# Performance work log

Measured on AMD Instinct MI355X. Metric: run time of the kernel, lower is better.

The kernel has to match this reference:

```python
import jax, jax.numpy as jnp
import numpy as np

B, D, L, H, P, IMG = 32, 768, 12, 12, 16, 224
N = (IMG // P) ** 2  # 196 patches
DH = D // H
FF = 4 * D
EPS = 1e-5


def _ln(x, w, b):
    m = jnp.mean(x, axis=-1, keepdims=True)
    v = jnp.mean((x - m) ** 2, axis=-1, keepdims=True)
    return (x - m) * jax.lax.rsqrt(v + EPS) * w + b


def setup_inputs() -> dict:
    key = jax.random.key(0)
    ks = jax.random.split(key, 12)
    s = 0.02
    return {
        "x": jax.random.normal(ks[0], (B, 3, IMG, IMG), jnp.float32),
        "patch_w": jax.random.normal(ks[1], (D, 3, P, P), jnp.float32) * s,
        "patch_b": jnp.zeros((D,), jnp.float32),
        "pos_embed": jax.random.normal(ks[2], (1, N, D), jnp.float32) * s,
        "ln1_w": jnp.ones((L, D), jnp.float32),
        "ln1_b": jnp.zeros((L, D), jnp.float32),
        "qkv_w": jax.random.normal(ks[3], (L, 3 * D, D), jnp.float32) * s,
        "qkv_b": jnp.zeros((L, 3 * D), jnp.float32),
        "proj_w": jax.random.normal(ks[4], (L, D, D), jnp.float32) * s,
        "proj_b": jnp.zeros((L, D), jnp.float32),
        "ln2_w": jnp.ones((L, D), jnp.float32),
        "ln2_b": jnp.zeros((L, D), jnp.float32),
        "fc1_w": jax.random.normal(ks[5], (L, FF, D), jnp.float32) * s,
        "fc1_b": jnp.zeros((L, FF), jnp.float32),
        "fc2_w": jax.random.normal(ks[6], (L, D, FF), jnp.float32) * s,
        "fc2_b": jnp.zeros((L, D), jnp.float32),
        "lnf_w": jnp.ones((D,), jnp.float32),
        "lnf_b": jnp.zeros((D,), jnp.float32),
    }


def reference(x, patch_w, patch_b, pos_embed, ln1_w, ln1_b, qkv_w, qkv_b,
              proj_w, proj_b, ln2_w, ln2_b, fc1_w, fc1_b, fc2_w, fc2_b,
              lnf_w, lnf_b):
    # Patch embed: strided conv, NCHW / OIHW
    h = jax.lax.conv_general_dilated(
        x, patch_w, window_strides=(P, P), padding="VALID",
        dimension_numbers=("NCHW", "OIHW", "NCHW")) + patch_b[None, :, None, None]
    b = h.shape[0]
    h = h.reshape(b, D, -1).transpose(0, 2, 1)  # (B, N, D)
    h = h + pos_embed  # broadcast over batch

    scale = DH ** (-0.5)
    for i in range(L):
        # --- attention (indices=None path: plain masked-free softmax) ---
        y = _ln(h, ln1_w[i], ln1_b[i])
        qkv = y @ qkv_w[i].T + qkv_b[i]                      # (B, N, 3D)
        qkv = qkv.reshape(b, -1, 3, H, DH).transpose(2, 0, 3, 1, 4)
        q, k, v = qkv[0], qkv[1], qkv[2]                     # (B, H, N, DH)
        attn = jax.nn.softmax(jnp.einsum("bhnd,bhmd->bhnm", q, k) * scale, axis=-1)
        o = jnp.einsum("bhnm,bhmd->bhnd", attn, v)
        o = o.transpose(0, 2, 1, 3).reshape(b, -1, D)
        h = h + (o @ proj_w[i].T + proj_b[i])
        # --- MLP ---
        y = _ln(h, ln2_w[i], ln2_b[i])
        y = jax.nn.gelu(y @ fc1_w[i].T + fc1_b[i], approximate=False)
        h = h + (y @ fc2_w[i].T + fc2_b[i])

    return _ln(h, lnf_w, lnf_b)
```

## Files before the change

kernel.cpp:

```cpp
#include <hip/hip_runtime.h>
#include <hip/hip_bf16.h>
#include <math.h>

#define BB    32
#define DD    768
#define LL    12
#define HH    12
#define NN    196
#define DHH   64
#define FFF   3072
#define MM    (BB * NN)
#define BHH   (BB * HH)

typedef float  floatx4 __attribute__((ext_vector_type(4)));
typedef __bf16 bf16x8  __attribute__((ext_vector_type(8)));

#define DEV __device__ __forceinline__

DEV unsigned short bf16u(float v) {
  __hip_bfloat16 h = __float2bfloat16(v);
  return __builtin_bit_cast(unsigned short, h);
}

DEV floatx4 mfma_bf16(bf16x8 a, bf16x8 b, floatx4 c) {
  return __builtin_amdgcn_mfma_f32_16x16x32_bf16(a, b, c, 0, 0, 0);
}

DEV void gl2lds16(const void* g, void* l) {
  __builtin_amdgcn_global_load_lds(
      (const __attribute__((address_space(1))) void*)g,
      (__attribute__((address_space(3))) void*)l, 16, 0, 0);
}

DEV float gelu_f(float v) {
  float ax = fabsf(v) * 0.70710678118654752f;
  float t = 1.0f / (1.0f + 0.3275911f * ax);
  float poly = t * (0.254829592f +
              t * (-0.284496736f +
              t * (1.421413741f +
              t * (-1.453152027f +
              t * 1.061405429f))));
  float er = 1.0f - poly * __expf(-ax * ax);
  er = (v < 0.0f) ? -er : er;
  return 0.5f * v * (1.0f + er);
}

DEV int xcd_swz(int orig, int nwg) {
  int q = nwg >> 3, r = nwg & 7;
  int xcd = orig & 7, pos = orig >> 3;
  int base = (xcd < r) ? xcd * (q + 1) : r * (q + 1) + (xcd - r) * q;
  return base + pos;
}

__global__ __launch_bounds__(256) void cvt4_k(const float4* __restrict__ in,
                                              ushort4* __restrict__ out, int n4) {
  int i = blockIdx.x * 256 + threadIdx.x;
  if (i < n4) {
    float4 v = in[i];
    ushort4 o;
    o.x = bf16u(v.x); o.y = bf16u(v.y); o.z = bf16u(v.z); o.w = bf16u(v.w);
    out[i] = o;
  }
}

__global__ __launch_bounds__(256) void im2col_k(const float* __restrict__ x,
                                                unsigned short* __restrict__ A) {
  int idx = blockIdx.x * 256 + threadIdx.x;
  int col = idx % DD;
  int token = idx / DD;
  int b = token / NN, p = token % NN;
  int pr = p / 14, pc = p % 14;
  int c = col >> 8, rm = col & 255, i = rm >> 4, j = rm & 15;
  float v = x[(((size_t)b * 3 + c) * 224 + pr * 16 + i) * 224 + pc * 16 + j];
  A[idx] = bf16u(v);
}

__global__ __launch_bounds__(256) void ln_k(const float* __restrict__ x,
                                            const float* __restrict__ w,
                                            const float* __restrict__ bb,
                                            unsigned short* __restrict__ outp) {
  const int token = blockIdx.x, tid = threadIdx.x;
  const float* xr = x + (size_t)token * DD;
  float v0 = xr[tid], v1 = xr[tid + 256], v2 = xr[tid + 512];
  float s = v0 + v1 + v2;
  float ss = v0 * v0 + v1 * v1 + v2 * v2;
#pragma unroll
  for (int off = 32; off; off >>= 1) {
    s += __shfl_down(s, off);
    ss += __shfl_down(ss, off);
  }
  __shared__ float rs[4], rq[4];
  if ((tid & 63) == 0) { rs[tid >> 6] = s; rq[tid >> 6] = ss; }
  __syncthreads();
  float tot = rs[0] + rs[1] + rs[2] + rs[3];
  float tq  = rq[0] + rq[1] + rq[2] + rq[3];
  const float mean = tot * (1.0f / 768.0f);
  const float var  = tq * (1.0f / 768.0f) - mean * mean;
  const float rstd = rsqrtf(var + 1e-5f);
#pragma unroll
  for (int t = 0; t < 3; t++) {
    int col = tid + t * 256;
    float xv = (t == 0) ? v0 : (t == 1 ? v1 : v2);
    float yv = (xv - mean) * rstd * w[col] + bb[col];
    outp[(size_t)token * DD + col] = bf16u(yv);
  }
}

template <int FINAL>
__global__ __launch_bounds__(256) void ln_fuse_k(float* __restrict__ h,
    const float* __restrict__ p0, const float* __restrict__ p1,
    const float* __restrict__ w, const float* __restrict__ bb,
    void* __restrict__ outp) {
  const int token = blockIdx.x, tid = threadIdx.x;
  const size_t base = (size_t)token * DD;
  float v[3];
#pragma unroll
  for (int t = 0; t < 3; t++) {
    const int col = tid + t * 256;
    v[t] = h[base + col] + p0[base + col] + p1[base + col];
    if (!FINAL) h[base + col] = v[t];
  }
  float s = v[0] + v[1] + v[2];
  float ss = v[0] * v[0] + v[1] * v[1] + v[2] * v[2];
#pragma unroll
  for (int off = 32; off; off >>= 1) {
    s += __shfl_down(s, off);
    ss += __shfl_down(ss, off);
  }
  __shared__ float rs[4], rq[4];
  if ((tid & 63) == 0) { rs[tid >> 6] = s; rq[tid >> 6] = ss; }
  __syncthreads();
  float tot = rs[0] + rs[1] + rs[2] + rs[3];
  float tq  = rq[0] + rq[1] + rq[2] + rq[3];
  const float mean = tot * (1.0f / 768.0f);
  const float var  = tq * (1.0f / 768.0f) - mean * mean;
  const float rstd = rsqrtf(var + 1e-5f);
#pragma unroll
  for (int t = 0; t < 3; t++) {
    const int col = tid + t * 256;
    float yv = (v[t] - mean) * rstd * w[col] + bb[col];
    if (FINAL) ((float*)outp)[base + col] = yv;
    else       ((unsigned short*)outp)[base + col] = bf16u(yv);
  }
}


template <int MODE>
__global__ __launch_bounds__(256, 4) void gemm_bt(
    const unsigned short* __restrict__ A, const unsigned short* __restrict__ W,
    const float* __restrict__ bias, void* __restrict__ outp, int K, int Nn) {
  __shared__ unsigned short smem[16384];
  unsigned short* As0 = smem;
  unsigned short* Bs0 = smem + 8192;
  const int tid = threadIdx.x;
  const int wave = tid >> 6, lane = tid & 63;
  const int nwg = gridDim.x * gridDim.y;
  const int wg = xcd_swz(blockIdx.x + gridDim.x * blockIdx.y, nwg);
  const int tm = (wg / gridDim.x) * 128, tn = (wg % gridDim.x) * 128;
  const int wm = (wave >> 1) * 64, wn = (wave & 1) * 64;
  const int lr = lane & 15, kq = lane >> 4;
  const int sw = (lr >> 1) & 3;
  const int koff = (kq ^ sw) * 8;
  const int c0 = tid, c1 = tid + 256;
  const int r0 = c0 >> 2, r1 = c1 >> 2;
  const int kc0 = ((c0 & 3) ^ ((r0 >> 1) & 3)) * 8;
  const int kc1 = ((c1 & 3) ^ ((r1 >> 1) & 3)) * 8;
  const size_t ga0 = (size_t)(tm + r0) * K + kc0;
  const size_t ga1 = (size_t)(tm + r1) * K + kc1;
  const size_t gb0 = (size_t)(tn + r0) * K + kc0;
  const size_t gb1 = (size_t)(tn + r1) * K + kc1;
  floatx4 acc[4][4] = {};
  auto stage = [&](int buf, int k0) {
    gl2lds16(A + ga0 + k0, As0 + buf * 4096 + c0 * 8);
    gl2lds16(A + ga1 + k0, As0 + buf * 4096 + c1 * 8);
    gl2lds16(W + gb0 + k0, Bs0 + buf * 4096 + c0 * 8);
    gl2lds16(W + gb1 + k0, Bs0 + buf * 4096 + c1 * 8);
  };
  const int nk = K >> 5;
  stage(0, 0);
  for (int it = 0; it < nk; it++) {
    const int cur = it & 1;
    __syncthreads();
    if (it + 1 < nk) stage(cur ^ 1, (it + 1) << 5);
    bf16x8 af[4], bq[4];
#pragma unroll
    for (int mi = 0; mi < 4; mi++)
      af[mi] = *(const bf16x8*)&As0[cur * 4096 + (wm + mi * 16 + lr) * 32 + koff];
#pragma unroll
    for (int ni = 0; ni < 4; ni++)
      bq[ni] = *(const bf16x8*)&Bs0[cur * 4096 + (wn + ni * 16 + lr) * 32 + koff];
#pragma unroll
    for (int mi = 0; mi < 4; mi++)
#pragma unroll
      for (int ni = 0; ni < 4; ni++)
        acc[mi][ni] = mfma_bf16(af[mi], bq[ni], acc[mi][ni]);
  }
  __syncthreads();
#pragma unroll
  for (int ni = 0; ni < 4; ni++) {
    const int lcol = wn + ni * 16 + lr;
    const float bv = bias[tn + lcol];
#pragma unroll
    for (int mi = 0; mi < 4; mi++) {
#pragma unroll
      for (int r = 0; r < 4; r++) {
        const int lrow = wm + mi * 16 + (lane >> 4) * 4 + r;
        float v = acc[mi][ni][r] + bv;
        if (MODE == 3) v = gelu_f(v);
        smem[lrow * 128 + lcol] = bf16u(v);
      }
    }
  }
  __syncthreads();
  const int tr = tid >> 4;
  const int tc = (tid & 15) * 8;
#pragma unroll
  for (int p = 0; p < 8; p++) {
    const int lrow = p * 16 + tr;
    uint4 d = *(const uint4*)&smem[lrow * 128 + tc];
    *(uint4*)&((unsigned short*)outp)[(size_t)(tm + lrow) * Nn + tn + tc] = d;
  }
}

__global__ __launch_bounds__(256, 4) void gemm_sk(
    const unsigned short* __restrict__ A, const unsigned short* __restrict__ W,
    const float* __restrict__ bias, float* __restrict__ p0,
    float* __restrict__ p1, int K, int Nn) {
  __shared__ unsigned short As[2][128 * 32];
  __shared__ unsigned short Bs[2][128 * 32];
  const int tid = threadIdx.x;
  const int wave = tid >> 6, lane = tid & 63;
  const int nwg = gridDim.x * gridDim.y;
  const int wg = xcd_swz(blockIdx.x + gridDim.x * blockIdx.y, nwg);
  const int tm = (wg / gridDim.x) * 128, tn = (wg % gridDim.x) * 128;
  const int kz = blockIdx.z;
  const int kper = K >> 1;
  const int kbase = kz * kper;
  const int wm = (wave >> 1) * 64, wn = (wave & 1) * 64;
  const int lr = lane & 15, kq = lane >> 4;
  const int sw = (lr >> 1) & 3;
  const int koff = (kq ^ sw) * 8;
  const int c0 = tid, c1 = tid + 256;
  const int r0 = c0 >> 2, r1 = c1 >> 2;
  const int kc0 = ((c0 & 3) ^ ((r0 >> 1) & 3)) * 8;
  const int kc1 = ((c1 & 3) ^ ((r1 >> 1) & 3)) * 8;
  const size_t ga0 = (size_t)(tm + r0) * K + kc0 + kbase;
  const size_t ga1 = (size_t)(tm + r1) * K + kc1 + kbase;
  const size_t gb0 = (size_t)(tn + r0) * K + kc0 + kbase;
  const size_t gb1 = (size_t)(tn + r1) * K + kc1 + kbase;
  floatx4 acc[4][4] = {};
  auto stage = [&](int buf, int k0) {
    gl2lds16(A + ga0 + k0, &As[buf][c0 * 8]);
    gl2lds16(A + ga1 + k0, &As[buf][c1 * 8]);
    gl2lds16(W + gb0 + k0, &Bs[buf][c0 * 8]);
    gl2lds16(W + gb1 + k0, &Bs[buf][c1 * 8]);
  };
  const int nk = kper >> 5;
  stage(0, 0);
  for (int it = 0; it < nk; it++) {
    const int cur = it & 1;
    __syncthreads();
    if (it + 1 < nk) stage(cur ^ 1, (it + 1) << 5);
    bf16x8 af[4], bq[4];
#pragma unroll
    for (int mi = 0; mi < 4; mi++)
      af[mi] = *(const bf16x8*)&As[cur][(wm + mi * 16 + lr) * 32 + koff];
#pragma unroll
    for (int ni = 0; ni < 4; ni++)
      bq[ni] = *(const bf16x8*)&Bs[cur][(wn + ni * 16 + lr) * 32 + koff];
#pragma unroll
    for (int mi = 0; mi < 4; mi++)
#pragma unroll
      for (int ni = 0; ni < 4; ni++)
        acc[mi][ni] = mfma_bf16(af[mi], bq[ni], acc[mi][ni]);
  }
  float* __restrict__ po = kz ? p1 : p0;
  const int rbase = tm + wm + (lane >> 4) * 4;
  const int cbase = tn + wn + lr;
#pragma unroll
  for (int ni = 0; ni < 4; ni++) {
    const int col = cbase + ni * 16;
    const float bv = kz ? 0.0f : bias[col];
#pragma unroll
    for (int mi = 0; mi < 4; mi++) {
#pragma unroll
      for (int r = 0; r < 4; r++) {
        const int row = rbase + mi * 16 + r;
        po[(size_t)row * Nn + col] = acc[mi][ni][r] + bv;
      }
    }
  }
}

template <int MODE>
__global__ __launch_bounds__(256, 4) void gemm64_bt(
    const unsigned short* __restrict__ A, const unsigned short* __restrict__ W,
    const float* __restrict__ bias, const float* __restrict__ aux,
    float* __restrict__ outp, int K, int Nn) {
  __shared__ unsigned short As[2][64 * 32];
  __shared__ unsigned short Bs[2][128 * 32];
  const int tid = threadIdx.x;
  const int wave = tid >> 6, lane = tid & 63;
  const int tm = blockIdx.y * 64, tn = blockIdx.x * 128;
  const int wm = (wave >> 1) * 32, wn = (wave & 1) * 64;
  const int lr = lane & 15, kq = lane >> 4;
  const int sw = (lr >> 1) & 3;
  const int koff = (kq ^ sw) * 8;
  const int ra = tid >> 2;
  const int kca = ((tid & 3) ^ ((ra >> 1) & 3)) * 8;
  const int c0 = tid, c1 = tid + 256;
  const int r0 = c0 >> 2, r1 = c1 >> 2;
  const int kc0 = ((c0 & 3) ^ ((r0 >> 1) & 3)) * 8;
  const int kc1 = ((c1 & 3) ^ ((r1 >> 1) & 3)) * 8;
  const size_t ga  = (size_t)(tm + ra) * K + kca;
  const size_t gb0 = (size_t)(tn + r0) * K + kc0;
  const size_t gb1 = (size_t)(tn + r1) * K + kc1;
  floatx4 acc[2][4] = {};
  auto stage = [&](int buf, int k0) {
    gl2lds16(A + ga + k0, &As[buf][tid * 8]);
    gl2lds16(W + gb0 + k0, &Bs[buf][c0 * 8]);
    gl2lds16(W + gb1 + k0, &Bs[buf][c1 * 8]);
  };
  const int nk = K >> 5;
  stage(0, 0);
  for (int it = 0; it < nk; it++) {
    const int cur = it & 1;
    __syncthreads();
    if (it + 1 < nk) stage(cur ^ 1, (it + 1) << 5);
    bf16x8 af[2], bq[4];
#pragma unroll
    for (int mi = 0; mi < 2; mi++)
      af[mi] = *(const bf16x8*)&As[cur][(wm + mi * 16 + lr) * 32 + koff];
#pragma unroll
    for (int ni = 0; ni < 4; ni++)
      bq[ni] = *(const bf16x8*)&Bs[cur][(wn + ni * 16 + lr) * 32 + koff];
#pragma unroll
    for (int mi = 0; mi < 2; mi++)
#pragma unroll
      for (int ni = 0; ni < 4; ni++)
        acc[mi][ni] = mfma_bf16(af[mi], bq[ni], acc[mi][ni]);
  }
  const int rbase = tm + wm + (lane >> 4) * 4;
  const int cbase = tn + wn + lr;
#pragma unroll
  for (int ni = 0; ni < 4; ni++) {
    const int col = cbase + ni * 16;
    const float bv = bias[col];
#pragma unroll
    for (int mi = 0; mi < 2; mi++) {
#pragma unroll
      for (int r = 0; r < 4; r++) {
        const int row = rbase + mi * 16 + r;
        float v = acc[mi][ni][r] + bv;
        float* hp = outp + (size_t)row * Nn + col;
        if (MODE == 1) *hp = v + aux[(size_t)(row % NN) * Nn + col];
        else           *hp = *hp + v;
      }
    }
  }
}

__global__ __launch_bounds__(256) void attn_fused_k(
    const unsigned short* __restrict__ qkv, const unsigned short* __restrict__ Vt,
    unsigned short* __restrict__ o) {
  __shared__ float S[32][232];
  __shared__ __align__(16) unsigned short Pl[32][232];
  const int tid = threadIdx.x;
  const int bh = blockIdx.x;
  const int b = bh / HH, hh = bh % HH;
  const int i0 = blockIdx.y * 32;
  const int wave = tid >> 6, lane = tid & 63;
  const int lr = lane & 15, k8 = (lane >> 4) * 8;
  for (int t = wave; t < 28; t += 4) {
    const int til = (t / 14) * 16, tj = (t % 14) * 16;
    const int iq = min(i0 + til + lr, NN - 1), jk = min(tj + lr, NN - 1);
    const unsigned short* qb = qkv + (size_t)(b * NN + iq) * 2304 + hh * 64 + k8;
    const unsigned short* kb = qkv + (size_t)(b * NN + jk) * 2304 + 768 + hh * 64 + k8;
    floatx4 acc = {0.f, 0.f, 0.f, 0.f};
    acc = mfma_bf16(*(const bf16x8*)qb, *(const bf16x8*)kb, acc);
    acc = mfma_bf16(*(const bf16x8*)(qb + 32), *(const bf16x8*)(kb + 32), acc);
#pragma unroll
    for (int r = 0; r < 4; r++)
      S[til + (lane >> 4) * 4 + r][tj + lr] = acc[r] * 0.125f;
  }
  __syncthreads();
  const int row = tid >> 3, sub = tid & 7;
  float v[28];
  float m = -1e30f;
#pragma unroll
  for (int t = 0; t < 28; t++) {
    const int c = sub + t * 8;
    v[t] = (c < NN) ? S[row][c] : -1e30f;
    m = fmaxf(m, v[t]);
  }
  m = fmaxf(m, __shfl_xor(m, 1));
  m = fmaxf(m, __shfl_xor(m, 2));
  m = fmaxf(m, __shfl_xor(m, 4));
  float s = 0.f;
#pragma unroll
  for (int t = 0; t < 28; t++) {
    v[t] = (sub + t * 8 < NN) ? __expf(v[t] - m) : 0.f;
    s += v[t];
  }
  s += __shfl_xor(s, 1);
  s += __shfl_xor(s, 2);
  s += __shfl_xor(s, 4);
  const float inv = 1.0f / s;
#pragma unroll
  for (int t = 0; t < 28; t++) Pl[row][sub + t * 8] = bf16u(v[t] * inv);
  __syncthreads();
#pragma unroll
  for (int w = 0; w < 2; w++) {
    const int tt = wave * 2 + w;
    const int it = tt >> 2, dt = tt & 3;
    const unsigned short* vb = Vt + ((size_t)bh * 64 + dt * 16 + lr) * 224 + k8;
    floatx4 acc = {0.f, 0.f, 0.f, 0.f};
#pragma unroll
    for (int k0 = 0; k0 < 224; k0 += 32)
      acc = mfma_bf16(*(const bf16x8*)&Pl[it * 16 + lr][k8 + k0],
                      *(const bf16x8*)(vb + k0), acc);
#pragma unroll
    for (int r = 0; r < 4; r++) {
      const int i = i0 + it * 16 + (lane >> 4) * 4 + r;
      if (i < NN)
        o[(size_t)(b * NN + i) * DD + hh * 64 + dt * 16 + lr] = bf16u(acc[r]);
    }
  }
}

__global__ __launch_bounds__(256) void vt_k(const unsigned short* __restrict__ qkv,
                                            unsigned short* __restrict__ Vt) {
  int idx = blockIdx.x * 256 + threadIdx.x;
  int j = idx % 224;
  int rest = idx / 224;
  int d = rest % 64, bh = rest / 64;
  int b = bh / HH, hh = bh % HH;
  unsigned short val = 0;
  if (j < NN) val = qkv[(size_t)(b * NN + j) * 2304 + 1536 + hh * 64 + d];
  Vt[idx] = val;
}

extern "C" void kernel_launch(void* const* d_in, const int* in_sizes, int n_in,
                              void* d_out, int out_size, void* d_ws, size_t ws_size,
                              hipStream_t stream) {
  const float* x       = (const float*)d_in[0];
  const float* patchw  = (const float*)d_in[1];
  const float* patchb  = (const float*)d_in[2];
  const float* pos     = (const float*)d_in[3];
  const float* ln1w    = (const float*)d_in[4];
  const float* ln1b    = (const float*)d_in[5];
  const float* qkvw    = (const float*)d_in[6];
  const float* qkvb    = (const float*)d_in[7];
  const float* projw   = (const float*)d_in[8];
  const float* projb   = (const float*)d_in[9];
  const float* ln2w    = (const float*)d_in[10];
  const float* ln2b    = (const float*)d_in[11];
  const float* fc1w    = (const float*)d_in[12];
  const float* fc1b    = (const float*)d_in[13];
  const float* fc2w    = (const float*)d_in[14];
  const float* fc2b    = (const float*)d_in[15];
  const float* lnfw    = (const float*)d_in[16];
  const float* lnfb    = (const float*)d_in[17];

  char* base = (char*)d_ws;
  size_t off = 0;
  auto alloc = [&](size_t bytes) {
    void* p = base + off;
    off = (off + bytes + 255) & ~(size_t)255;
    return p;
  };
  unsigned short* Wq  = (unsigned short*)alloc((size_t)LL * 2304 * 768 * 2);
  unsigned short* Wp  = (unsigned short*)alloc((size_t)LL * 768 * 768 * 2);
  unsigned short* W1  = (unsigned short*)alloc((size_t)LL * 3072 * 768 * 2);
  unsigned short* W2  = (unsigned short*)alloc((size_t)LL * 768 * 3072 * 2);
  unsigned short* Wpe = (unsigned short*)alloc((size_t)768 * 768 * 2);
  float*          h   = (float*)alloc((size_t)MM * DD * 4);
  unsigned short* y   = (unsigned short*)alloc((size_t)MM * DD * 2);
  unsigned short* qkv = (unsigned short*)alloc((size_t)MM * 2304 * 2);
  unsigned short* g   = (unsigned short*)alloc((size_t)MM * FFF * 2);
  float*          pp1 = (float*)alloc((size_t)MM * DD * 4);
  unsigned short* Vt  = (unsigned short*)alloc((size_t)BHH * 64 * 224 * 2);
  unsigned short* o   = (unsigned short*)alloc((size_t)MM * DD * 2);
  if (off > ws_size) return;

  unsigned short* Aim = qkv;
  float* pp0 = (float*)qkv;

  auto cvt = [&](const float* src, unsigned short* dst, size_t n) {
    int n4 = (int)(n / 4);
    cvt4_k<<<dim3((n4 + 255) / 256), dim3(256), 0, stream>>>(
        (const float4*)src, (ushort4*)dst, n4);
  };
  cvt(qkvw, Wq, (size_t)LL * 2304 * 768);
  cvt(projw, Wp, (size_t)LL * 768 * 768);
  cvt(fc1w, W1, (size_t)LL * 3072 * 768);
  cvt(fc2w, W2, (size_t)LL * 768 * 3072);
  cvt(patchw, Wpe, (size_t)768 * 768);

  im2col_k<<<dim3(MM * DD / 256), dim3(256), 0, stream>>>(x, Aim);
  gemm64_bt<1><<<dim3(6, 98), dim3(256), 0, stream>>>(Aim, Wpe, patchb, pos, h, 768, 768);

  ln_k<<<dim3(MM), dim3(256), 0, stream>>>(h, ln1w, ln1b, y);

  for (int l = 0; l < LL; l++) {
    gemm_bt<0><<<dim3(18, 49), dim3(256), 0, stream>>>(
        y, Wq + (size_t)l * 2304 * 768, qkvb + l * 2304, qkv, 768, 2304);
    vt_k<<<dim3(BHH * 64 * 224 / 256), dim3(256), 0, stream>>>(qkv, Vt);
    attn_fused_k<<<dim3(BHH, 7), dim3(256), 0, stream>>>(qkv, Vt, o);
    gemm_sk<<<dim3(6, 49, 2), dim3(256), 0, stream>>>(
        o, Wp + (size_t)l * 768 * 768, projb + l * 768, pp0, pp1, 768, 768);
    ln_fuse_k<0><<<dim3(MM), dim3(256), 0, stream>>>(
        h, pp0, pp1, ln2w + l * 768, ln2b + l * 768, y);
    gemm_bt<3><<<dim3(24, 49), dim3(256), 0, stream>>>(
        y, W1 + (size_t)l * 3072 * 768, fc1b + l * 3072, g, 768, 3072);
    gemm_sk<<<dim3(6, 49, 2), dim3(256), 0, stream>>>(
        g, W2 + (size_t)l * 768 * 3072, fc2b + l * 768, pp0, pp1, 3072, 768);
    if (l + 1 < LL) {
      ln_fuse_k<0><<<dim3(MM), dim3(256), 0, stream>>>(
          h, pp0, pp1, ln1w + (l + 1) * 768, ln1b + (l + 1) * 768, y);
    } else {
      ln_fuse_k<1><<<dim3(MM), dim3(256), 0, stream>>>(
          h, pp0, pp1, lnfw, lnfb, d_out);
    }
  }
}
```

Measured before the change: 3.347 ms.

## Fuse V transpose into QKV GEMM epilogue and use wave-per-token layernorm

The QKV GEMM gains a mode whose V-column tiles are transposed in shared memory and written straight into the padded Vt buffer. This removes the separate vt_k transpose kernel each layer, and the zero padding is written once up front. The layernorm kernels now give each token to one wave with float4 loads and xor-shuffle reductions, dropping the shared-memory reduction and block barrier. The trade-offs are a larger LDS footprint in the GEMM, scattered stores for tiles that cross batch boundaries, and partial-qkv writes skipped for V tiles.

```diff
diff --git a/kernel.cpp b/kernel.cpp
--- a/kernel.cpp
+++ b/kernel.cpp
@@ -75,34 +75,49 @@
   A[idx] = bf16u(v);
 }
 
-__global__ __launch_bounds__(256) void ln_k(const float* __restrict__ x,
-                                            const float* __restrict__ w,
-                                            const float* __restrict__ bb,
-                                            unsigned short* __restrict__ outp) {
-  const int token = blockIdx.x, tid = threadIdx.x;
-  const float* xr = x + (size_t)token * DD;
-  float v0 = xr[tid], v1 = xr[tid + 256], v2 = xr[tid + 512];
-  float s = v0 + v1 + v2;
-  float ss = v0 * v0 + v1 * v1 + v2 * v2;
+__global__ __launch_bounds__(256) void vtpad_k(unsigned short* __restrict__ Vt) {
+  int idx = blockIdx.x * 256 + threadIdx.x;
+  int jj = idx % 28, rest = idx / 28;
+  Vt[(size_t)rest * 224 + 196 + jj] = 0;
+}
+
+__global__ __launch_bounds__(256) void lnw_k(const float* __restrict__ x,
+                                             const float* __restrict__ w,
+                                             const float* __restrict__ bb,
+                                             unsigned short* __restrict__ outp) {
+  const int token = blockIdx.x * 4 + (threadIdx.x >> 6);
+  const int lane = threadIdx.x & 63;
+  const size_t base = (size_t)token * DD;
+  const float4* x4 = (const float4*)(x + base);
+  const float4* w4 = (const float4*)w;
+  const float4* b4 = (const float4*)bb;
+  float4 v[3];
+  float s = 0.f, ss = 0.f;
+#pragma unroll
+  for (int j = 0; j < 3; j++) {
+    float4 t = x4[lane + j * 64];
+    v[j] = t;
+    s += t.x + t.y + t.z + t.w;
+    ss += t.x * t.x + t.y * t.y + t.z * t.z + t.w * t.w;
+  }
 #pragma unroll
   for (int off = 32; off; off >>= 1) {
-    s += __shfl_down(s, off);
-    ss += __shfl_down(ss, off);
-  }
-  __shared__ float rs[4], rq[4];
-  if ((tid & 63) == 0) { rs[tid >> 6] = s; rq[tid >> 6] = ss; }
-  __syncthreads();
-  float tot = rs[0] + rs[1] + rs[2] + rs[3];
-  float tq  = rq[0] + rq[1] + rq[2] + rq[3];
-  const float mean = tot * (1.0f / 768.0f);
-  const float var  = tq * (1.0f / 768.0f) - mean * mean;
+    s += __shfl_xor(s, off);
+    ss += __shfl_xor(ss, off);
+  }
+  const float mean = s * (1.0f / 768.0f);
+  const float var  = ss * (1.0f / 768.0f) - mean * mean;
   const float rstd = rsqrtf(var + 1e-5f);
 #pragma unroll
-  for (int t = 0; t < 3; t++) {
-    int col = tid + t * 256;
-    float xv = (t == 0) ? v0 : (t == 1 ? v1 : v2);
-    float yv = (xv - mean) * rstd * w[col] + bb[col];
-    outp[(size_t)token * DD + col] = bf16u(yv);
+  for (int j = 0; j < 3; j++) {
+    const int c4 = lane + j * 64;
+    float4 wv = w4[c4], bv = b4[c4];
+    ushort4 o;
+    o.x = bf16u((v[j].x - mean) * rstd * wv.x + bv.x);
+    o.y = bf16u((v[j].y - mean) * rstd * wv.y + bv.y);
+    o.z = bf16u((v[j].z - mean) * rstd * wv.z + bv.z);
+    o.w = bf16u((v[j].w - mean) * rstd * wv.w + bv.w);
+    ((ushort4*)((unsigned short*)outp + base))[c4] = o;
   }
 }
 
@@ -111,36 +126,52 @@
     const float* __restrict__ p0, const float* __restrict__ p1,
     const float* __restrict__ w, const float* __restrict__ bb,
     void* __restrict__ outp) {
-  const int token = blockIdx.x, tid = threadIdx.x;
+  const int token = blockIdx.x * 4 + (threadIdx.x >> 6);
+  const int lane = threadIdx.x & 63;
   const size_t base = (size_t)token * DD;
-  float v[3];
-#pragma unroll
-  for (int t = 0; t < 3; t++) {
-    const int col = tid + t * 256;
-    v[t] = h[base + col] + p0[base + col] + p1[base + col];
-    if (!FINAL) h[base + col] = v[t];
-  }
-  float s = v[0] + v[1] + v[2];
-  float ss = v[0] * v[0] + v[1] * v[1] + v[2] * v[2];
+  const float4* h4 = (const float4*)(h + base);
+  const float4* p04 = (const float4*)(p0 + base);
+  const float4* p14 = (const float4*)(p1 + base);
+  const float4* w4 = (const float4*)w;
+  const float4* b4 = (const float4*)bb;
+  float4 v[3];
+  float s = 0.f, ss = 0.f;
+#pragma unroll
+  for (int j = 0; j < 3; j++) {
+    const int c4 = lane + j * 64;
+    float4 a = h4[c4], b2 = p04[c4], c2 = p14[c4];
+    float4 t;
+    t.x = a.x + b2.x + c2.x; t.y = a.y + b2.y + c2.y;
+    t.z = a.z + b2.z + c2.z; t.w = a.w + b2.w + c2.w;
+    v[j] = t;
+    s += t.x + t.y + t.z + t.w;
+    ss += t.x * t.x + t.y * t.y + t.z * t.z + t.w * t.w;
+    if (!FINAL) ((float4*)(h + base))[c4] = t;
+  }
 #pragma unroll
   for (int off = 32; off; off >>= 1) {
-    s += __shfl_down(s, off);
-    ss += __shfl_down(ss, off);
-  }
-  __shared__ float rs[4], rq[4];
-  if ((tid & 63) == 0) { rs[tid >> 6] = s; rq[tid >> 6] = ss; }
-  __syncthreads();
-  float tot = rs[0] + rs[1] + rs[2] + rs[3];
-  float tq  = rq[0] + rq[1] + rq[2] + rq[3];
-  const float mean = tot * (1.0f / 768.0f);
-  const float var  = tq * (1.0f / 768.0f) - mean * mean;
+    s += __shfl_xor(s, off);
+    ss += __shfl_xor(ss, off);
+  }
+  const float mean = s * (1.0f / 768.0f);
+  const float var  = ss * (1.0f / 768.0f) - mean * mean;
   const float rstd = rsqrtf(var + 1e-5f);
 #pragma unroll
-  for (int t = 0; t < 3; t++) {
-    const int col = tid + t * 256;
-    float yv = (v[t] - mean) * rstd * w[col] + bb[col];
-    if (FINAL) ((float*)outp)[base + col] = yv;
-    else       ((unsigned short*)outp)[base + col] = bf16u(yv);
+  for (int j = 0; j < 3; j++) {
+    const int c4 = lane + j * 64;
+    float4 wv = w4[c4], bv = b4[c4];
+    float4 yv;
+    yv.x = (v[j].x - mean) * rstd * wv.x + bv.x;
+    yv.y = (v[j].y - mean) * rstd * wv.y + bv.y;
+    yv.z = (v[j].z - mean) * rstd * wv.z + bv.z;
+    yv.w = (v[j].w - mean) * rstd * wv.w + bv.w;
+    if (FINAL) {
+      ((float4*)((float*)outp + base))[c4] = yv;
+    } else {
+      ushort4 o;
+      o.x = bf16u(yv.x); o.y = bf16u(yv.y); o.z = bf16u(yv.z); o.w = bf16u(yv.w);
+      ((ushort4*)((unsigned short*)outp + base))[c4] = o;
+    }
   }
 }
 
@@ -148,8 +179,9 @@
 template <int MODE>
 __global__ __launch_bounds__(256, 4) void gemm_bt(
     const unsigned short* __restrict__ A, const unsigned short* __restrict__ W,
-    const float* __restrict__ bias, void* __restrict__ outp, int K, int Nn) {
-  __shared__ unsigned short smem[16384];
+    const float* __restrict__ bias, void* __restrict__ outp,
+    unsigned short* __restrict__ vtp, int K, int Nn) {
+  __shared__ unsigned short smem[17408];
   unsigned short* As0 = smem;
   unsigned short* Bs0 = smem + 8192;
   const int tid = threadIdx.x;
@@ -196,29 +228,68 @@
         acc[mi][ni] = mfma_bf16(af[mi], bq[ni], acc[mi][ni]);
   }
   __syncthreads();
-#pragma unroll
-  for (int ni = 0; ni < 4; ni++) {
-    const int lcol = wn + ni * 16 + lr;
-    const float bv = bias[tn + lcol];
-#pragma unroll
-    for (int mi = 0; mi < 4; mi++) {
-#pragma unroll
-      for (int r = 0; r < 4; r++) {
-        const int lrow = wm + mi * 16 + (lane >> 4) * 4 + r;
-        float v = acc[mi][ni][r] + bv;
-        if (MODE == 3) v = gelu_f(v);
-        smem[lrow * 128 + lcol] = bf16u(v);
+  const bool vtile = (MODE == 4) && (tn >= 1536);
+  if (vtile) {
+#pragma unroll
+    for (int ni = 0; ni < 4; ni++) {
+      const int lcol = wn + ni * 16 + lr;
+      const float bv = bias[tn + lcol];
+#pragma unroll
+      for (int mi = 0; mi < 4; mi++) {
+#pragma unroll
+        for (int r = 0; r < 4; r++) {
+          const int lrow = wm + mi * 16 + (lane >> 4) * 4 + r;
+          smem[lcol * 136 + lrow] = bf16u(acc[mi][ni][r] + bv);
+        }
       }
     }
-  }
-  __syncthreads();
-  const int tr = tid >> 4;
-  const int tc = (tid & 15) * 8;
-#pragma unroll
-  for (int p = 0; p < 8; p++) {
-    const int lrow = p * 16 + tr;
-    uint4 d = *(const uint4*)&smem[lrow * 128 + tc];
-    *(uint4*)&((unsigned short*)outp)[(size_t)(tm + lrow) * Nn + tn + tc] = d;
+    __syncthreads();
+    const int vbase = tn - 1536;
+#pragma unroll
+    for (int sch = 0; sch < 8; sch++) {
+      const int c = tid + sch * 256;
+      const int col = c >> 4, j0 = (c & 15) * 8;
+      const int hh = (vbase + col) >> 6, d = (vbase + col) & 63;
+      const int row0 = tm + j0;
+      const int b0 = row0 / NN, jA = row0 % NN;
+      if (jA + 7 < NN) {
+        unsigned short* dst = vtp + ((size_t)(b0 * HH + hh) * 64 + d) * 224 + jA;
+        *(ushort4*)dst = *(const ushort4*)&smem[col * 136 + j0];
+        *(ushort4*)(dst + 4) = *(const ushort4*)&smem[col * 136 + j0 + 4];
+      } else {
+#pragma unroll
+        for (int k = 0; k < 8; k++) {
+          const int row = row0 + k;
+          const int b = row / NN, j = row % NN;
+          vtp[((size_t)(b * HH + hh) * 64 + d) * 224 + j] = smem[col * 136 + j0 + k];
+        }
+      }
+    }
+  } else {
+#pragma unroll
+    for (int ni = 0; ni < 4; ni++) {
+      const int lcol = wn + ni * 16 + lr;
+      const float bv = bias[tn + lcol];
+#pragma unroll
+      for (int mi = 0; mi < 4; mi++) {
+#pragma unroll
+        for (int r = 0; r < 4; r++) {
+          const int lrow = wm + mi * 16 + (lane >> 4) * 4 + r;
+          float v = acc[mi][ni][r] + bv;
+          if (MODE == 3) v = gelu_f(v);
+          smem[lrow * 128 + lcol] = bf16u(v);
+        }
+      }
+    }
+    __syncthreads();
+    const int tr = tid >> 4;
+    const int tc = (tid & 15) * 8;
+#pragma unroll
+    for (int p = 0; p < 8; p++) {
+      const int lrow = p * 16 + tr;
+      uint4 dv = *(const uint4*)&smem[lrow * 128 + tc];
+      *(uint4*)&((unsigned short*)outp)[(size_t)(tm + lrow) * Nn + tn + tc] = dv;
+    }
   }
 }
 
@@ -428,18 +499,6 @@
   }
 }
 
-__global__ __launch_bounds__(256) void vt_k(const unsigned short* __restrict__ qkv,
-                                            unsigned short* __restrict__ Vt) {
-  int idx = blockIdx.x * 256 + threadIdx.x;
-  int j = idx % 224;
-  int rest = idx / 224;
-  int d = rest % 64, bh = rest / 64;
-  int b = bh / HH, hh = bh % HH;
-  unsigned short val = 0;
-  if (j < NN) val = qkv[(size_t)(b * NN + j) * 2304 + 1536 + hh * 64 + d];
-  Vt[idx] = val;
-}
-
 extern "C" void kernel_launch(void* const* d_in, const int* in_sizes, int n_in,
                               void* d_out, int out_size, void* d_ws, size_t ws_size,
                               hipStream_t stream) {
@@ -497,29 +556,30 @@
   cvt(fc2w, W2, (size_t)LL * 768 * 3072);
   cvt(patchw, Wpe, (size_t)768 * 768);
 
+  vtpad_k<<<dim3(BHH * 64 * 28 / 256), dim3(256), 0, stream>>>(Vt);
+
   im2col_k<<<dim3(MM * DD / 256), dim3(256), 0, stream>>>(x, Aim);
   gemm64_bt<1><<<dim3(6, 98), dim3(256), 0, stream>>>(Aim, Wpe, patchb, pos, h, 768, 768);
 
-  ln_k<<<dim3(MM), dim3(256), 0, stream>>>(h, ln1w, ln1b, y);
+  lnw_k<<<dim3(MM / 4), dim3(256), 0, stream>>>(h, ln1w, ln1b, y);
 
   for (int l = 0; l < LL; l++) {
-    gemm_bt<0><<<dim3(18, 49), dim3(256), 0, stream>>>(
-        y, Wq + (size_t)l * 2304 * 768, qkvb + l * 2304, qkv, 768, 2304);
-    vt_k<<<dim3(BHH * 64 * 224 / 256), dim3(256), 0, stream>>>(qkv, Vt);
+    gemm_bt<4><<<dim3(18, 49), dim3(256), 0, stream>>>(
+        y, Wq + (size_t)l * 2304 * 768, qkvb + l * 2304, qkv, Vt, 768, 2304);
     attn_fused_k<<<dim3(BHH, 7), dim3(256), 0, stream>>>(qkv, Vt, o);
     gemm_sk<<<dim3(6, 49, 2), dim3(256), 0, stream>>>(
         o, Wp + (size_t)l * 768 * 768, projb + l * 768, pp0, pp1, 768, 768);
-    ln_fuse_k<0><<<dim3(MM), dim3(256), 0, stream>>>(
+    ln_fuse_k<0><<<dim3(MM / 4), dim3(256), 0, stream>>>(
         h, pp0, pp1, ln2w + l * 768, ln2b + l * 768, y);
     gemm_bt<3><<<dim3(24, 49), dim3(256), 0, stream>>>(
-        y, W1 + (size_t)l * 3072 * 768, fc1b + l * 3072, g, 768, 3072);
+        y, W1 + (size_t)l * 3072 * 768, fc1b + l * 3072, g, nullptr, 768, 3072);
     gemm_sk<<<dim3(6, 49, 2), dim3(256), 0, stream>>>(
         g, W2 + (size_t)l * 768 * 3072, fc2b + l * 768, pp0, pp1, 3072, 768);
     if (l + 1 < LL) {
-      ln_fuse_k<0><<<dim3(MM), dim3(256), 0, stream>>>(
+      ln_fuse_k<0><<<dim3(MM / 4), dim3(256), 0, stream>>>(
           h, pp0, pp1, ln1w + (l + 1) * 768, ln1b + (l + 1) * 768, y);
     } else {
-      ln_fuse_k<1><<<dim3(MM), dim3(256), 0, stream>>>(
+      ln_fuse_k<1><<<dim3(MM / 4), dim3(256), 0, stream>>>(
           h, pp0, pp1, lnfw, lnfb, d_out);
     }
   }
```

Result: faster. 3.141 ms (-6.2%).
